# Kernel optimization log

Hardware: AMD Instinct MI355X
Metric: run time of the kernel (lower is better)

The kernel has to match this reference:

```python
import jax, jax.numpy as jnp
import numpy as np

WORD_DIM = 200
ASPECT_DIM = 32
NUM_NEG = 2
AVG_RATING = 3.8
LR_RATING = 1.0
LR_ABAE = 1.0


def setup_inputs() -> dict:
    key = jax.random.key(0)
    ks = jax.random.split(key, 20)
    R, L, D, A, B, NNZ = 20000, 30, WORD_DIM, ASPECT_DIM, 4096, 65536
    e_w = jax.random.normal(ks[0], (R, L, D), jnp.float32)
    y_s = jax.random.normal(ks[1], (R, D), jnp.float32)
    z_n = jax.random.normal(ks[2], (R * NUM_NEG, D), jnp.float32)
    label = jax.random.uniform(ks[3], (B,), jnp.float32, 1.0, 5.0)
    u_idx = jnp.stack([jax.random.randint(ks[4], (NNZ,), 0, B),
                       jax.random.randint(ks[5], (NNZ,), 0, R)]).astype(jnp.int64)
    i_idx = jnp.stack([jax.random.randint(ks[6], (NNZ,), 0, B),
                       jax.random.randint(ks[7], (NNZ,), 0, R)]).astype(jnp.int64)
    u_val = jax.random.uniform(ks[8], (NNZ,), jnp.float32)
    i_val = jax.random.uniform(ks[9], (NNZ,), jnp.float32)
    s = 0.05
    M_w = jax.random.normal(ks[10], (D, D), jnp.float32) * s
    M_b = jnp.zeros((D,), jnp.float32)
    W_w = jax.random.normal(ks[11], (A, D), jnp.float32) * s
    W_b = jnp.zeros((A,), jnp.float32)
    T_w = jax.random.normal(ks[12], (D, A), jnp.float32) * s
    T_b = jnp.zeros((D,), jnp.float32)
    fc_w = jax.random.uniform(ks[13], (1, A), jnp.float32, -0.05, 0.05)
    fc_b = jnp.zeros((1,), jnp.float32)
    fm_V = jax.random.uniform(ks[14], (A, 10), jnp.float32, -0.05, 0.05)
    return dict(e_w=e_w, y_s=y_s, z_n=z_n, label=label,
                user_histor_value=u_val, item_histor_value=i_val,
                M_w=M_w, M_b=M_b, W_w=W_w, W_b=W_b, T_w=T_w, T_b=T_b,
                fc_w=fc_w, fc_b=fc_b, fm_V=fm_V,
                user_histor_index=u_idx, item_histor_index=i_idx)


def _l2norm(x, axis):
    return x / jnp.maximum(jnp.linalg.norm(x, axis=axis, keepdims=True), 1e-12)


def reference(e_w, y_s, z_n, label, user_histor_value, item_histor_value,
              M_w, M_b, W_w, W_b, T_w, T_b, fc_w, fc_b, fm_V,
              user_histor_index, item_histor_index):
    R, L, D = e_w.shape
    A = W_w.shape[0]
    B = label.shape[0]
    # ABAE attention: dx = (e_w @ M^T + b) . y_s  -> (R, L)
    Me = jnp.einsum('rld,ed->rle', e_w, M_w) + M_b  # (R, L, D)
    dx = jnp.einsum('rld,rd->rl', Me, y_s)
    ax = jax.nn.softmax(dx, axis=1)                 # attention over words
    z_s = jnp.einsum('rld,rl->rd', e_w, ax)         # (R, D) weighted sentence emb
    p_t = z_s @ W_w.T + W_b                         # (R, A) aspect weights
    r_s = p_t @ T_w.T + T_b                         # (R, D) reconstructed emb
    # margin ranking (hinge) loss on cosine similarities
    c1 = jnp.sum(_l2norm(r_s, 1) * _l2norm(z_s, 1), axis=-1, keepdims=True)  # (R,1)
    c1 = jnp.tile(c1, (1, NUM_NEG)).reshape(-1)                              # (R*neg,)
    zn = _l2norm(z_n.reshape(R, NUM_NEG, D), 2)
    c2 = jnp.sum(zn * _l2norm(r_s, 1)[:, None, :], axis=-1).reshape(-1)
    abae_out_loss = jnp.maximum(0.0, 1.0 - (c1 - c2))
    J_loss = jnp.mean(abae_out_loss)
    # orthogonality regularizer on aspect matrix columns
    Tn = _l2norm(T_w, 0)                            # normalize each column (dim=0)
    G = Tn.T @ Tn                                   # (A, A)
    U_loss = jnp.mean((G - jnp.eye(A, dtype=G.dtype)) ** 2)
    abae_loss = U_loss + J_loss
    # sparse pooling: (B, R) sparse @ (R, A)
    u_rows, u_cols = user_histor_index[0], user_histor_index[1]
    i_rows, i_cols = item_histor_index[0], item_histor_index[1]
    user_aspect = jax.ops.segment_sum(p_t[u_cols] * user_histor_value[:, None],
                                      u_rows, num_segments=B)
    item_aspect = jax.ops.segment_sum(p_t[i_cols] * item_histor_value[:, None],
                                      i_rows, num_segments=B)
    output_emb = user_aspect * item_aspect          # (B, A)
    # factorization machine
    fm_linear = output_emb @ fc_w.T + fc_b          # (B, 1)
    i1 = (output_emb @ fm_V) ** 2
    i2 = (output_emb ** 2) @ (fm_V ** 2)
    # NOTE: faithful to source -- the 0.5*sum reduces over ALL elements (scalar)
    fm_output = 0.5 * jnp.sum(i1 - i2) + fm_linear  # (B, 1)
    prediction = fm_output + jnp.float32(AVG_RATING)
    rating_out_loss = (prediction.reshape(-1) - label) ** 2
    rating_loss = jnp.mean(rating_out_loss)
    obj = LR_RATING * rating_loss + LR_ABAE * abae_loss
    return (obj, rating_out_loss, abae_out_loss, prediction, user_aspect, item_aspect)
```

## Files before the change

kernel.cpp:

```cpp
#include <hip/hip_runtime.h>
#include <hip/hip_bf16.h>
#include <math.h>

#define R_CNT   20000
#define L_CNT   30
#define D_CNT   200
#define A_CNT   32
#define B_CNT   4096
#define NNZ_CNT 65536
#define AVG_RATING 3.8f

#define KA_GRID 1536

#define OUT_OBJ  0
#define OUT_RL   1
#define OUT_AB   (1 + B_CNT)
#define OUT_PRED (OUT_AB + 2*R_CNT)
#define OUT_UA   (OUT_PRED + B_CNT)
#define OUT_IA   (OUT_UA + B_CNT*A_CNT)

#define WS_DBL    0
#define WS_MODE   32
#define WS_FMLIN  64
#define WS_PT     16448
#define WS_V      2576448
#define WS_JPART  18627648
#define WS_SPART  18667648
#define WS_UPART  18671744

#define BAR_LDS() do { asm volatile("s_waitcnt lgkmcnt(0)" ::: "memory"); \
                       __builtin_amdgcn_s_barrier(); \
                       __builtin_amdgcn_sched_barrier(0); } while (0)
#define BAR_FULL() do { asm volatile("s_waitcnt vmcnt(0) lgkmcnt(0)" ::: "memory"); \
                        __builtin_amdgcn_s_barrier(); \
                        __builtin_amdgcn_sched_barrier(0); } while (0)

__device__ __forceinline__ float4 blk_reduce4(float4 v, float4* scratch) {
    __syncthreads();
    #pragma unroll
    for (int o = 32; o >= 1; o >>= 1) {
        v.x += __shfl_xor(v.x, o);
        v.y += __shfl_xor(v.y, o);
        v.z += __shfl_xor(v.z, o);
        v.w += __shfl_xor(v.w, o);
    }
    int w = threadIdx.x >> 6;
    if ((threadIdx.x & 63) == 0) scratch[w] = v;
    __syncthreads();
    float4 t0 = scratch[0], t1 = scratch[1], t2 = scratch[2], t3 = scratch[3];
    return make_float4(t0.x + t1.x + t2.x + t3.x,
                       t0.y + t1.y + t2.y + t3.y,
                       t0.z + t1.z + t2.z + t3.z,
                       t0.w + t1.w + t2.w + t3.w);
}

__global__ __launch_bounds__(256) void k_pre(const float* __restrict__ y_s,
                                             const float* __restrict__ M_w,
                                             const float* __restrict__ T_w,
                                             const int* __restrict__ u_idx,
                                             float* __restrict__ V,
                                             float* __restrict__ upart,
                                             float* __restrict__ out,
                                             double* __restrict__ dbl,
                                             int* __restrict__ mode) {
    __shared__ __align__(16) float sh[8224];
    const int tid = threadIdx.x;
    const int bid = blockIdx.x;

    if (bid < 313) {
        float* Msh = sh;
        float* Ysh = sh + 6500;
        int r0 = bid * 64;
        int dg = tid & 31, rg = tid >> 5;
        float acc[8][8];
        #pragma unroll
        for (int i = 0; i < 8; i++)
            #pragma unroll
            for (int j = 0; j < 8; j++) acc[i][j] = 0.f;
        for (int e0 = 0; e0 < D_CNT; e0 += 25) {
            __syncthreads();
            for (int idx = tid; idx < 25 * 256; idx += 256) {
                int ee = idx >> 8, d = idx & 255;
                Msh[ee * 260 + d] = (d < D_CNT) ? M_w[(e0 + ee) * D_CNT + d] : 0.f;
            }
            for (int idx = tid; idx < 25 * 64; idx += 256) {
                int rr = idx / 25, ee = idx - rr * 25;
                int row = r0 + rr;
                Ysh[ee * 68 + rr] = (row < R_CNT) ? y_s[row * D_CNT + e0 + ee] : 0.f;
            }
            __syncthreads();
            for (int ee = 0; ee < 25; ee++) {
                const float4 ya = *(const float4*)&Ysh[ee * 68 + rg * 8];
                const float4 yb = *(const float4*)&Ysh[ee * 68 + rg * 8 + 4];
                const float4 ma = *(const float4*)&Msh[ee * 260 + dg * 8];
                const float4 mb = *(const float4*)&Msh[ee * 260 + dg * 8 + 4];
                float ys[8] = {ya.x, ya.y, ya.z, ya.w, yb.x, yb.y, yb.z, yb.w};
                float ms[8] = {ma.x, ma.y, ma.z, ma.w, mb.x, mb.y, mb.z, mb.w};
                #pragma unroll
                for (int i = 0; i < 8; i++)
                    #pragma unroll
                    for (int j = 0; j < 8; j++)
                        acc[i][j] = fmaf(ys[i], ms[j], acc[i][j]);
            }
        }
        if (dg < 25) {
            #pragma unroll
            for (int i = 0; i < 8; i++) {
                int row = r0 + rg * 8 + i;
                if (row < R_CNT) {
                    *(float4*)&V[row * D_CNT + dg * 8]     = make_float4(acc[i][0], acc[i][1], acc[i][2], acc[i][3]);
                    *(float4*)&V[row * D_CNT + dg * 8 + 4] = make_float4(acc[i][4], acc[i][5], acc[i][6], acc[i][7]);
                }
            }
        }
    } else if (bid < 345) {
        float* Tsh = sh;
        float* tn  = sh + 6400;
        float4* red4 = (float4*)(sh + 6448);
        for (int idx = tid; idx < 1600; idx += 256)
            ((float4*)Tsh)[idx] = ((const float4*)T_w)[idx];
        __syncthreads();
        int a = tid >> 3, k = tid & 7;
        float p = 0.f;
        #pragma unroll
        for (int j = 0; j < 25; ++j) { float t = Tsh[(k + 8*j)*32 + a]; p = fmaf(t, t, p); }
        p += __shfl_xor(p, 1); p += __shfl_xor(p, 2); p += __shfl_xor(p, 4);
        if (k == 0) tn[a] = fmaxf(sqrtf(p), 1e-12f);
        __syncthreads();
        const int i = bid - 313;
        float s = 0.f;
        #pragma unroll
        for (int j = 0; j < 25; ++j)
            s = fmaf(Tsh[(k + 8*j)*32 + i], Tsh[(k + 8*j)*32 + a], s);
        s += __shfl_xor(s, 1); s += __shfl_xor(s, 2); s += __shfl_xor(s, 4);
        float part = 0.f;
        if (k == 0) {
            float g = s / (tn[i] * tn[a]);
            float diff = g - ((i == a) ? 1.f : 0.f);
            part = diff * diff;
        }
        float4 tot = blk_reduce4(make_float4(part, 0.f, 0.f, 0.f), red4);
        if (tid == 0) upart[i] = tot.x;
    } else {
        int base = (bid - 345) * 2048;
        #pragma unroll
        for (int j = 0; j < 8; ++j)
            out[OUT_UA + base + j * 256 + tid] = 0.f;
        if (bid == 345 && tid == 0) {
            dbl[0] = 0.0; dbl[1] = 0.0; dbl[2] = 0.0;
            int m = 1;
            for (int i = 1; i < 256; i += 2) if (u_idx[i] != 0) { m = 0; break; }
            *mode = m;
        }
    }
}

__device__ __forceinline__ void stage_E(const float* __restrict__ ew_src,
                                        float* ldsE, int w, int lane) {
    #pragma unroll
    for (int i = 0; i < 6; ++i) {
        int c = w * 6 + i;
        int f4 = c * 64 + lane;
        if (f4 > 1499) f4 = 1499;
        __builtin_amdgcn_global_load_lds(
            (const __attribute__((address_space(1))) unsigned int*)(ew_src + (size_t)f4 * 4),
            (__attribute__((address_space(3))) unsigned int*)(ldsE + c * 256),
            16, 0, 0);
    }
}
__device__ __forceinline__ void stage_V(const float* __restrict__ v_src,
                                        float* ldsV, int w, int lane) {
    __builtin_amdgcn_global_load_lds(
        (const __attribute__((address_space(1))) unsigned int*)(v_src + w * 64 + lane),
        (__attribute__((address_space(3))) unsigned int*)(ldsV + w * 64),
        4, 0, 0);
}

__global__ __launch_bounds__(256, 6) void k_attn(const float* __restrict__ e_w,
                                                 const float* __restrict__ V,
                                                 const float* __restrict__ z_n,
                                                 const float* __restrict__ W_w,
                                                 const float* __restrict__ W_b,
                                                 const float* __restrict__ T_w,
                                                 const float* __restrict__ T_b,
                                                 float* __restrict__ p_t,
                                                 float* __restrict__ out,
                                                 double* __restrict__ jpart) {
    __shared__ __align__(16) float bufE[6144];
    __shared__ __align__(16) float bufV[256];
    __shared__ __align__(16) float zsh[D_CNT];
    __shared__ float axs[32], pts[32];
    __shared__ float4 red[8];
    const int tid = threadIdx.x;
    const int w = tid >> 6, lane = tid & 63;
    const float wb = W_b[tid >> 3];
    const float tb = (tid < D_CNT) ? T_b[tid] : 0.f;
    double jloc = 0.0;

    int r = blockIdx.x;
    stage_E(e_w + (size_t)r * 6000, bufE, w, lane);
    stage_V(V + (size_t)r * D_CNT, bufV, w, lane);
    __syncthreads();

    for (;;) {
        const int rn = r + KA_GRID;
        const bool have_next = (rn < R_CNT);

        float zn0 = 0.f, zn1 = 0.f;
        if (tid < D_CNT) {
            zn0 = z_n[(size_t)(2 * r) * D_CNT + tid];
            zn1 = z_n[(size_t)(2 * r + 1) * D_CNT + tid];
        }

        if (tid < 240) {
            int l = tid >> 3, k = tid & 7;
            float p = 0.f;
            #pragma unroll
            for (int j = 0; j < 25; ++j)
                p = fmaf(bufE[l * 200 + k + 8 * j], bufV[k + 8 * j], p);
            p += __shfl_xor(p, 1); p += __shfl_xor(p, 2); p += __shfl_xor(p, 4);
            if (k == 0) axs[l] = p;
        }
        BAR_LDS();

        if (tid < 64) {
            float v = (tid < L_CNT) ? axs[tid] : -3.0e38f;
            float m = v;
            #pragma unroll
            for (int o = 32; o >= 1; o >>= 1) m = fmaxf(m, __shfl_xor(m, o));
            float e = (tid < L_CNT) ? __expf(v - m) : 0.f;
            float s = e;
            #pragma unroll
            for (int o = 32; o >= 1; o >>= 1) s += __shfl_xor(s, o);
            if (tid < L_CNT) axs[tid] = e / s;
        }
        BAR_LDS();

        float zreg = 0.f;
        if (tid < D_CNT) {
            #pragma unroll
            for (int l = 0; l < L_CNT; ++l)
                zreg = fmaf(bufE[l * 200 + tid], axs[l], zreg);
            zsh[tid] = zreg;
        }
        BAR_LDS();

        if (have_next) {
            stage_E(e_w + (size_t)rn * 6000, bufE, w, lane);
            stage_V(V + (size_t)rn * D_CNT, bufV, w, lane);
        }

        {
            int a = tid >> 3, k = tid & 7;
            float p = 0.f;
            #pragma unroll
            for (int j = 0; j < 25; ++j)
                p = fmaf(zsh[k + 8 * j], W_w[a * 200 + k + 8 * j], p);
            p += __shfl_xor(p, 1); p += __shfl_xor(p, 2); p += __shfl_xor(p, 4);
            if (k == 0) {
                float pt = p + wb;
                pts[a] = pt;
                p_t[(size_t)r * 32 + a] = pt;
            }
        }
        BAR_LDS();

        float rv = 0.f;
        if (tid < D_CNT) {
            rv = tb;
            const float4* tw = (const float4*)(T_w + tid * 32);
            #pragma unroll
            for (int q = 0; q < 8; ++q) {
                float4 t = tw[q];
                rv = fmaf(t.x, pts[4 * q + 0], rv);
                rv = fmaf(t.y, pts[4 * q + 1], rv);
                rv = fmaf(t.z, pts[4 * q + 2], rv);
                rv = fmaf(t.w, pts[4 * q + 3], rv);
            }
        }
        float4 Av = make_float4(rv * rv, rv * zreg, zreg * zreg, zn0 * zn0);
        float4 Bv = make_float4(zn0 * rv, zn1 * zn1, zn1 * rv, 0.f);
        #pragma unroll
        for (int o = 32; o >= 1; o >>= 1) {
            Av.x += __shfl_xor(Av.x, o); Av.y += __shfl_xor(Av.y, o);
            Av.z += __shfl_xor(Av.z, o); Av.w += __shfl_xor(Av.w, o);
            Bv.x += __shfl_xor(Bv.x, o); Bv.y += __shfl_xor(Bv.y, o);
            Bv.z += __shfl_xor(Bv.z, o);
        }
        if ((tid & 63) == 0) { red[2 * w] = Av; red[2 * w + 1] = Bv; }

        BAR_FULL();

        if (tid == 0) {
            float rr = 0.f, rz = 0.f, zz = 0.f, n00 = 0.f, n0r = 0.f, n11 = 0.f, n1r = 0.f;
            #pragma unroll
            for (int i = 0; i < 4; ++i) {
                float4 a = red[2 * i], b = red[2 * i + 1];
                rr += a.x; rz += a.y; zz += a.z; n00 += a.w;
                n0r += b.x; n11 += b.y; n1r += b.z;
            }
            float nr = fmaxf(sqrtf(rr), 1e-12f);
            float nz = fmaxf(sqrtf(zz), 1e-12f);
            float c1  = rz  / (nr * nz);
            float c20 = n0r / (fmaxf(sqrtf(n00), 1e-12f) * nr);
            float c21 = n1r / (fmaxf(sqrtf(n11), 1e-12f) * nr);
            float l0 = fmaxf(0.f, 1.f - (c1 - c20));
            float l1 = fmaxf(0.f, 1.f - (c1 - c21));
            out[OUT_AB + 2 * r]     = l0;
            out[OUT_AB + 2 * r + 1] = l1;
            jloc += (double)l0 + (double)l1;
        }
        if (!have_next) break;
        r = rn;
    }
    if (tid == 0) jpart[blockIdx.x] = jloc;
}

__global__ __launch_bounds__(256) void k_scatter(const int* __restrict__ u_idx,
                                                 const int* __restrict__ i_idx,
                                                 const float* __restrict__ u_val,
                                                 const float* __restrict__ i_val,
                                                 const float* __restrict__ p_t,
                                                 const int* __restrict__ mode,
                                                 float* __restrict__ out) {
    long long gid = (long long)blockIdx.x * 256 + threadIdx.x;
    const long long HALF = (long long)NNZ_CNT * 32;
    int is_item = gid >= HALF;
    long long rem = gid - (is_item ? HALF : 0);
    int k = (int)(rem >> 5), a = (int)(rem & 31);
    const int* idx = is_item ? i_idx : u_idx;
    const float* val = is_item ? i_val : u_val;
    int m64 = *mode;
    int row, col;
    if (m64) { row = idx[2 * k]; col = idx[2 * (NNZ_CNT + k)]; }
    else     { row = idx[k];     col = idx[NNZ_CNT + k]; }
    float v = p_t[col * 32 + a] * val[k];
    float* base = out + (is_item ? OUT_IA : OUT_UA);
    atomicAdd(&base[row * 32 + a], v);
}

__global__ __launch_bounds__(256) void k_fm(const float* __restrict__ out,
                                            const float* __restrict__ fc_w,
                                            const float* __restrict__ fc_b,
                                            const float* __restrict__ fm_V,
                                            float* __restrict__ fm_lin,
                                            double* __restrict__ spart) {
    __shared__ float parts[8];
    int tid = threadIdx.x;
    int a = tid & 31;
    int b = blockIdx.x * 8 + (tid >> 5);
    float ua = out[OUT_UA + b * 32 + a];
    float ia = out[OUT_IA + b * 32 + a];
    float oe = ua * ia;
    float oe2 = oe * oe;
    float lin = oe * fc_w[a];
    #pragma unroll
    for (int o = 1; o < 32; o <<= 1) lin += __shfl_xor(lin, o);
    float part = 0.f;
    #pragma unroll
    for (int j = 0; j < 10; j++) {
        float v = fm_V[a * 10 + j];
        float s1 = oe * v;
        float s2 = oe2 * v * v;
        #pragma unroll
        for (int o = 1; o < 32; o <<= 1) { s1 += __shfl_xor(s1, o); s2 += __shfl_xor(s2, o); }
        part += s1 * s1 - s2;
    }
    if (a == 0) {
        fm_lin[b] = lin + fc_b[0];
        parts[tid >> 5] = part;
    }
    __syncthreads();
    if (tid == 0) {
        float s = 0.f;
        #pragma unroll
        for (int i = 0; i < 8; ++i) s += parts[i];
        spart[blockIdx.x] = 0.5 * (double)s;
    }
}

__global__ __launch_bounds__(256) void k_predfinal(const float* __restrict__ label,
                                                   const float* __restrict__ fm_lin,
                                                   const double* __restrict__ spart,
                                                   const double* __restrict__ jpart,
                                                   const float* __restrict__ upart,
                                                   float* __restrict__ out) {
    __shared__ double dred[4];
    __shared__ float Ssh;
    int tid = threadIdx.x;
    double sl = spart[tid] + spart[tid + 256];
    #pragma unroll
    for (int o = 32; o >= 1; o >>= 1) sl += __shfl_xor(sl, o);
    if ((tid & 63) == 0) dred[tid >> 6] = sl;
    __syncthreads();
    if (tid == 0) Ssh = (float)(dred[0] + dred[1] + dred[2] + dred[3]);
    __syncthreads();
    float S = Ssh;
    double racc = 0.0;
    #pragma unroll
    for (int i = 0; i < 16; ++i) {
        int b = tid + 256 * i;
        float pred = fm_lin[b] + S + AVG_RATING;
        float d = pred - label[b];
        float rl = d * d;
        out[OUT_PRED + b] = pred;
        out[OUT_RL + b] = rl;
        racc += (double)rl;
    }
    double jacc = 0.0;
    for (int i = tid; i < KA_GRID; i += 256) jacc += jpart[i];
    float u = (tid < 32) ? upart[tid] : 0.f;
    #pragma unroll
    for (int o = 32; o >= 1; o >>= 1) {
        racc += __shfl_xor(racc, o);
        jacc += __shfl_xor(jacc, o);
        u    += __shfl_xor(u, o);
    }
    __syncthreads();
    if ((tid & 63) == 0) dred[tid >> 6] = racc;
    __syncthreads();
    double rsum = dred[0] + dred[1] + dred[2] + dred[3];
    __syncthreads();
    if ((tid & 63) == 0) dred[tid >> 6] = jacc;
    __syncthreads();
    double jsum = dred[0] + dred[1] + dred[2] + dred[3];
    __shared__ float ured[4];
    if ((tid & 63) == 0) ured[tid >> 6] = u;
    __syncthreads();
    if (tid == 0) {
        double U = (double)(ured[0] + ured[1] + ured[2] + ured[3]) / 1024.0;
        double J = jsum / (2.0 * R_CNT);
        double RL = rsum / (double)B_CNT;
        out[OUT_OBJ] = (float)(RL + U + J);
    }
}

extern "C" void kernel_launch(void* const* d_in, const int* in_sizes, int n_in,
                              void* d_out, int out_size, void* d_ws, size_t ws_size,
                              hipStream_t stream) {
    const float* e_w   = (const float*)d_in[0];
    const float* y_s   = (const float*)d_in[1];
    const float* z_n   = (const float*)d_in[2];
    const float* label = (const float*)d_in[3];
    const float* u_val = (const float*)d_in[4];
    const float* i_val = (const float*)d_in[5];
    const float* M_w   = (const float*)d_in[6];
    const float* W_w   = (const float*)d_in[8];
    const float* W_b   = (const float*)d_in[9];
    const float* T_w   = (const float*)d_in[10];
    const float* T_b   = (const float*)d_in[11];
    const float* fc_w  = (const float*)d_in[12];
    const float* fc_b  = (const float*)d_in[13];
    const float* fm_V  = (const float*)d_in[14];
    const int*   u_idx = (const int*)d_in[15];
    const int*   i_idx = (const int*)d_in[16];

    float* out = (float*)d_out;
    char* ws = (char*)d_ws;
    double* dbl   = (double*)(ws + WS_DBL);
    int* mode     = (int*)(ws + WS_MODE);
    float* fm_lin = (float*)(ws + WS_FMLIN);
    float* p_t    = (float*)(ws + WS_PT);
    float* V      = (float*)(ws + WS_V);
    double* jpart = (double*)(ws + WS_JPART);
    double* spart = (double*)(ws + WS_SPART);
    float* upart  = (float*)(ws + WS_UPART);

    k_pre<<<473, 256, 0, stream>>>(y_s, M_w, T_w, u_idx, V, upart, out, dbl, mode);
    k_attn<<<KA_GRID, 256, 0, stream>>>(e_w, V, z_n, W_w, W_b, T_w, T_b,
                                        p_t, out, jpart);
    k_scatter<<<(2 * NNZ_CNT * 32) / 256, 256, 0, stream>>>(u_idx, i_idx, u_val, i_val,
                                                            p_t, mode, out);
    k_fm<<<B_CNT / 8, 256, 0, stream>>>(out, fc_w, fc_b, fm_V, fm_lin, spart);
    k_predfinal<<<1, 256, 0, stream>>>(label, fm_lin, spart, jpart, upart, out);
}
```

Baseline: 370.2 us.

## Split attention into streaming online-softmax kernel and batched tail kernel

Replaces the persistent LDS-staged attention kernel with two kernels. The first gives each 64-lane wave one review row: it streams e_w with float4 loads, prefetches the next two positions, and keeps an online softmax so the weighted sum is built in registers, overwriting V with z. The second kernel handles four rows per block for the W/T projections and the hinge loss, reusing each W_w load across the four rows. The aim is more concurrent memory traffic on the dominant e_w read, with fewer block barriers. The cost is an extra launch and a round trip of z through global memory, and only 50 of 64 lanes do useful work in the streaming kernel.

```diff
diff --git a/kernel.cpp b/kernel.cpp
--- a/kernel.cpp
+++ b/kernel.cpp
@@ -10,7 +10,8 @@
 #define NNZ_CNT 65536
 #define AVG_RATING 3.8f
 
-#define KA_GRID 1536
+#define FLASH_GRID 5000
+#define TAIL_GRID  5000
 
 #define OUT_OBJ  0
 #define OUT_RL   1
@@ -27,13 +28,6 @@
 #define WS_JPART  18627648
 #define WS_SPART  18667648
 #define WS_UPART  18671744
-
-#define BAR_LDS() do { asm volatile("s_waitcnt lgkmcnt(0)" ::: "memory"); \
-                       __builtin_amdgcn_s_barrier(); \
-                       __builtin_amdgcn_sched_barrier(0); } while (0)
-#define BAR_FULL() do { asm volatile("s_waitcnt vmcnt(0) lgkmcnt(0)" ::: "memory"); \
-                        __builtin_amdgcn_s_barrier(); \
-                        __builtin_amdgcn_sched_barrier(0); } while (0)
 
 __device__ __forceinline__ float4 blk_reduce4(float4 v, float4* scratch) {
     __syncthreads();
@@ -155,131 +149,136 @@
     }
 }
 
-__device__ __forceinline__ void stage_E(const float* __restrict__ ew_src,
-                                        float* ldsE, int w, int lane) {
-    #pragma unroll
-    for (int i = 0; i < 6; ++i) {
-        int c = w * 6 + i;
-        int f4 = c * 64 + lane;
-        if (f4 > 1499) f4 = 1499;
-        __builtin_amdgcn_global_load_lds(
-            (const __attribute__((address_space(1))) unsigned int*)(ew_src + (size_t)f4 * 4),
-            (__attribute__((address_space(3))) unsigned int*)(ldsE + c * 256),
-            16, 0, 0);
-    }
-}
-__device__ __forceinline__ void stage_V(const float* __restrict__ v_src,
-                                        float* ldsV, int w, int lane) {
-    __builtin_amdgcn_global_load_lds(
-        (const __attribute__((address_space(1))) unsigned int*)(v_src + w * 64 + lane),
-        (__attribute__((address_space(3))) unsigned int*)(ldsV + w * 64),
-        4, 0, 0);
-}
-
-__global__ __launch_bounds__(256, 6) void k_attn(const float* __restrict__ e_w,
-                                                 const float* __restrict__ V,
-                                                 const float* __restrict__ z_n,
-                                                 const float* __restrict__ W_w,
-                                                 const float* __restrict__ W_b,
-                                                 const float* __restrict__ T_w,
-                                                 const float* __restrict__ T_b,
-                                                 float* __restrict__ p_t,
-                                                 float* __restrict__ out,
-                                                 double* __restrict__ jpart) {
-    __shared__ __align__(16) float bufE[6144];
-    __shared__ __align__(16) float bufV[256];
-    __shared__ __align__(16) float zsh[D_CNT];
-    __shared__ float axs[32], pts[32];
+__global__ __launch_bounds__(256, 6) void k_flash(const float* __restrict__ e_w,
+                                                  float* __restrict__ V) {
+    const int lane = threadIdx.x & 63;
+    const int r = blockIdx.x * 4 + (threadIdx.x >> 6);
+    const bool act = lane < 50;
+    const int dl = act ? lane : 0;
+
+    const float4* ew4 = (const float4*)(e_w + (size_t)r * (L_CNT * D_CNT));
+    float4 v4 = ((const float4*)(V + (size_t)r * D_CNT))[dl];
+
+    float m = -3.0e38f, s = 0.f;
+    float4 zs = make_float4(0.f, 0.f, 0.f, 0.f);
+    float4 e0 = ew4[dl];
+    float4 e1 = ew4[50 + dl];
+    #pragma unroll
+    for (int l = 0; l < L_CNT; l += 2) {
+        float4 n0 = e0, n1 = e1;
+        if (l + 2 < L_CNT) {
+            n0 = ew4[(l + 2) * 50 + dl];
+            n1 = ew4[(l + 3) * 50 + dl];
+        }
+        float p0 = act ? (e0.x*v4.x + e0.y*v4.y + e0.z*v4.z + e0.w*v4.w) : 0.f;
+        float p1 = act ? (e1.x*v4.x + e1.y*v4.y + e1.z*v4.z + e1.w*v4.w) : 0.f;
+        #pragma unroll
+        for (int o = 1; o < 64; o <<= 1) {
+            p0 += __shfl_xor(p0, o);
+            p1 += __shfl_xor(p1, o);
+        }
+        float nm = fmaxf(m, fmaxf(p0, p1));
+        float sc = __expf(m - nm);
+        float w0 = __expf(p0 - nm);
+        float w1 = __expf(p1 - nm);
+        s = s * sc + w0 + w1;
+        zs.x = zs.x * sc + w0 * e0.x + w1 * e1.x;
+        zs.y = zs.y * sc + w0 * e0.y + w1 * e1.y;
+        zs.z = zs.z * sc + w0 * e0.z + w1 * e1.z;
+        zs.w = zs.w * sc + w0 * e0.w + w1 * e1.w;
+        m = nm;
+        e0 = n0; e1 = n1;
+    }
+    const float inv = 1.f / s;
+    zs.x *= inv; zs.y *= inv; zs.z *= inv; zs.w *= inv;
+    if (act) ((float4*)(V + (size_t)r * D_CNT))[lane] = zs;
+}
+
+__global__ __launch_bounds__(256) void k_tail(const float* __restrict__ zs,
+                                              const float* __restrict__ z_n,
+                                              const float* __restrict__ W_w,
+                                              const float* __restrict__ W_b,
+                                              const float* __restrict__ T_w,
+                                              const float* __restrict__ T_b,
+                                              float* __restrict__ p_t,
+                                              float* __restrict__ out,
+                                              double* __restrict__ jpart) {
+    __shared__ __align__(16) float zsh[4 * D_CNT];
+    __shared__ float pts[4 * 32];
     __shared__ float4 red[8];
     const int tid = threadIdx.x;
-    const int w = tid >> 6, lane = tid & 63;
-    const float wb = W_b[tid >> 3];
-    const float tb = (tid < D_CNT) ? T_b[tid] : 0.f;
+    const int w = tid >> 6;
+    const int r0 = blockIdx.x * 4;
+
+    for (int i = tid; i < 200; i += 256)
+        ((float4*)zsh)[i] = ((const float4*)(zs + (size_t)r0 * D_CNT))[i];
+
+    float zn[8];
+    #pragma unroll
+    for (int q = 0; q < 8; ++q) zn[q] = 0.f;
+    if (tid < D_CNT) {
+        #pragma unroll
+        for (int q = 0; q < 4; ++q) {
+            zn[2*q]   = z_n[(size_t)(2*(r0+q))     * D_CNT + tid];
+            zn[2*q+1] = z_n[(size_t)(2*(r0+q) + 1) * D_CNT + tid];
+        }
+    }
+    __syncthreads();
+
+    {
+        int a = tid >> 3, k = tid & 7;
+        float a0 = 0.f, a1 = 0.f, a2 = 0.f, a3 = 0.f;
+        #pragma unroll
+        for (int j = 0; j < 25; ++j) {
+            float wv = W_w[a * D_CNT + k + 8 * j];
+            a0 = fmaf(zsh[0*D_CNT + k + 8*j], wv, a0);
+            a1 = fmaf(zsh[1*D_CNT + k + 8*j], wv, a1);
+            a2 = fmaf(zsh[2*D_CNT + k + 8*j], wv, a2);
+            a3 = fmaf(zsh[3*D_CNT + k + 8*j], wv, a3);
+        }
+        #pragma unroll
+        for (int o = 1; o < 8; o <<= 1) {
+            a0 += __shfl_xor(a0, o); a1 += __shfl_xor(a1, o);
+            a2 += __shfl_xor(a2, o); a3 += __shfl_xor(a3, o);
+        }
+        if (k == 0) {
+            float wbv = W_b[a];
+            float p0 = a0 + wbv, p1 = a1 + wbv, p2 = a2 + wbv, p3 = a3 + wbv;
+            pts[0*32+a] = p0; pts[1*32+a] = p1; pts[2*32+a] = p2; pts[3*32+a] = p3;
+            p_t[(size_t)(r0+0) * 32 + a] = p0;
+            p_t[(size_t)(r0+1) * 32 + a] = p1;
+            p_t[(size_t)(r0+2) * 32 + a] = p2;
+            p_t[(size_t)(r0+3) * 32 + a] = p3;
+        }
+    }
+    __syncthreads();
+
+    float rv[4] = {0.f, 0.f, 0.f, 0.f};
+    float zv[4] = {0.f, 0.f, 0.f, 0.f};
+    if (tid < D_CNT) {
+        float tbv = T_b[tid];
+        rv[0] = tbv; rv[1] = tbv; rv[2] = tbv; rv[3] = tbv;
+        const float4* tw = (const float4*)(T_w + tid * 32);
+        #pragma unroll
+        for (int u = 0; u < 8; ++u) {
+            float4 t = tw[u];
+            #pragma unroll
+            for (int q = 0; q < 4; ++q) {
+                rv[q] = fmaf(t.x, pts[q*32 + 4*u + 0], rv[q]);
+                rv[q] = fmaf(t.y, pts[q*32 + 4*u + 1], rv[q]);
+                rv[q] = fmaf(t.z, pts[q*32 + 4*u + 2], rv[q]);
+                rv[q] = fmaf(t.w, pts[q*32 + 4*u + 3], rv[q]);
+            }
+        }
+        #pragma unroll
+        for (int q = 0; q < 4; ++q) zv[q] = zsh[q * D_CNT + tid];
+    }
+
     double jloc = 0.0;
-
-    int r = blockIdx.x;
-    stage_E(e_w + (size_t)r * 6000, bufE, w, lane);
-    stage_V(V + (size_t)r * D_CNT, bufV, w, lane);
-    __syncthreads();
-
-    for (;;) {
-        const int rn = r + KA_GRID;
-        const bool have_next = (rn < R_CNT);
-
-        float zn0 = 0.f, zn1 = 0.f;
-        if (tid < D_CNT) {
-            zn0 = z_n[(size_t)(2 * r) * D_CNT + tid];
-            zn1 = z_n[(size_t)(2 * r + 1) * D_CNT + tid];
-        }
-
-        if (tid < 240) {
-            int l = tid >> 3, k = tid & 7;
-            float p = 0.f;
-            #pragma unroll
-            for (int j = 0; j < 25; ++j)
-                p = fmaf(bufE[l * 200 + k + 8 * j], bufV[k + 8 * j], p);
-            p += __shfl_xor(p, 1); p += __shfl_xor(p, 2); p += __shfl_xor(p, 4);
-            if (k == 0) axs[l] = p;
-        }
-        BAR_LDS();
-
-        if (tid < 64) {
-            float v = (tid < L_CNT) ? axs[tid] : -3.0e38f;
-            float m = v;
-            #pragma unroll
-            for (int o = 32; o >= 1; o >>= 1) m = fmaxf(m, __shfl_xor(m, o));
-            float e = (tid < L_CNT) ? __expf(v - m) : 0.f;
-            float s = e;
-            #pragma unroll
-            for (int o = 32; o >= 1; o >>= 1) s += __shfl_xor(s, o);
-            if (tid < L_CNT) axs[tid] = e / s;
-        }
-        BAR_LDS();
-
-        float zreg = 0.f;
-        if (tid < D_CNT) {
-            #pragma unroll
-            for (int l = 0; l < L_CNT; ++l)
-                zreg = fmaf(bufE[l * 200 + tid], axs[l], zreg);
-            zsh[tid] = zreg;
-        }
-        BAR_LDS();
-
-        if (have_next) {
-            stage_E(e_w + (size_t)rn * 6000, bufE, w, lane);
-            stage_V(V + (size_t)rn * D_CNT, bufV, w, lane);
-        }
-
-        {
-            int a = tid >> 3, k = tid & 7;
-            float p = 0.f;
-            #pragma unroll
-            for (int j = 0; j < 25; ++j)
-                p = fmaf(zsh[k + 8 * j], W_w[a * 200 + k + 8 * j], p);
-            p += __shfl_xor(p, 1); p += __shfl_xor(p, 2); p += __shfl_xor(p, 4);
-            if (k == 0) {
-                float pt = p + wb;
-                pts[a] = pt;
-                p_t[(size_t)r * 32 + a] = pt;
-            }
-        }
-        BAR_LDS();
-
-        float rv = 0.f;
-        if (tid < D_CNT) {
-            rv = tb;
-            const float4* tw = (const float4*)(T_w + tid * 32);
-            #pragma unroll
-            for (int q = 0; q < 8; ++q) {
-                float4 t = tw[q];
-                rv = fmaf(t.x, pts[4 * q + 0], rv);
-                rv = fmaf(t.y, pts[4 * q + 1], rv);
-                rv = fmaf(t.z, pts[4 * q + 2], rv);
-                rv = fmaf(t.w, pts[4 * q + 3], rv);
-            }
-        }
-        float4 Av = make_float4(rv * rv, rv * zreg, zreg * zreg, zn0 * zn0);
-        float4 Bv = make_float4(zn0 * rv, zn1 * zn1, zn1 * rv, 0.f);
+    #pragma unroll
+    for (int q = 0; q < 4; ++q) {
+        float4 Av = make_float4(rv[q]*rv[q], rv[q]*zv[q], zv[q]*zv[q], zn[2*q]*zn[2*q]);
+        float4 Bv = make_float4(zn[2*q]*rv[q], zn[2*q+1]*zn[2*q+1], zn[2*q+1]*rv[q], 0.f);
         #pragma unroll
         for (int o = 32; o >= 1; o >>= 1) {
             Av.x += __shfl_xor(Av.x, o); Av.y += __shfl_xor(Av.y, o);
@@ -287,15 +286,13 @@
             Bv.x += __shfl_xor(Bv.x, o); Bv.y += __shfl_xor(Bv.y, o);
             Bv.z += __shfl_xor(Bv.z, o);
         }
-        if ((tid & 63) == 0) { red[2 * w] = Av; red[2 * w + 1] = Bv; }
-
-        BAR_FULL();
-
+        if ((tid & 63) == 0) { red[2*w] = Av; red[2*w+1] = Bv; }
+        __syncthreads();
         if (tid == 0) {
             float rr = 0.f, rz = 0.f, zz = 0.f, n00 = 0.f, n0r = 0.f, n11 = 0.f, n1r = 0.f;
             #pragma unroll
             for (int i = 0; i < 4; ++i) {
-                float4 a = red[2 * i], b = red[2 * i + 1];
+                float4 a = red[2*i], b = red[2*i+1];
                 rr += a.x; rz += a.y; zz += a.z; n00 += a.w;
                 n0r += b.x; n11 += b.y; n1r += b.z;
             }
@@ -306,12 +303,11 @@
             float c21 = n1r / (fmaxf(sqrtf(n11), 1e-12f) * nr);
             float l0 = fmaxf(0.f, 1.f - (c1 - c20));
             float l1 = fmaxf(0.f, 1.f - (c1 - c21));
-            out[OUT_AB + 2 * r]     = l0;
-            out[OUT_AB + 2 * r + 1] = l1;
+            out[OUT_AB + 2 * (r0 + q)]     = l0;
+            out[OUT_AB + 2 * (r0 + q) + 1] = l1;
             jloc += (double)l0 + (double)l1;
         }
-        if (!have_next) break;
-        r = rn;
+        __syncthreads();
     }
     if (tid == 0) jpart[blockIdx.x] = jloc;
 }
@@ -387,6 +383,7 @@
                                                    float* __restrict__ out) {
     __shared__ double dred[4];
     __shared__ float Ssh;
+    __shared__ float ured[4];
     int tid = threadIdx.x;
     double sl = spart[tid] + spart[tid + 256];
     #pragma unroll
@@ -408,7 +405,7 @@
         racc += (double)rl;
     }
     double jacc = 0.0;
-    for (int i = tid; i < KA_GRID; i += 256) jacc += jpart[i];
+    for (int i = tid; i < TAIL_GRID; i += 256) jacc += jpart[i];
     float u = (tid < 32) ? upart[tid] : 0.f;
     #pragma unroll
     for (int o = 32; o >= 1; o >>= 1) {
@@ -424,7 +421,6 @@
     if ((tid & 63) == 0) dred[tid >> 6] = jacc;
     __syncthreads();
     double jsum = dred[0] + dred[1] + dred[2] + dred[3];
-    __shared__ float ured[4];
     if ((tid & 63) == 0) ured[tid >> 6] = u;
     __syncthreads();
     if (tid == 0) {
@@ -467,8 +463,8 @@
     float* upart  = (float*)(ws + WS_UPART);
 
     k_pre<<<473, 256, 0, stream>>>(y_s, M_w, T_w, u_idx, V, upart, out, dbl, mode);
-    k_attn<<<KA_GRID, 256, 0, stream>>>(e_w, V, z_n, W_w, W_b, T_w, T_b,
-                                        p_t, out, jpart);
+    k_flash<<<FLASH_GRID, 256, 0, stream>>>(e_w, V);
+    k_tail<<<TAIL_GRID, 256, 0, stream>>>(V, z_n, W_w, W_b, T_w, T_b, p_t, out, jpart);
     k_scatter<<<(2 * NNZ_CNT * 32) / 256, 256, 0, stream>>>(u_idx, i_idx, u_val, i_val,
                                                             p_t, mode, out);
     k_fm<<<B_CNT / 8, 256, 0, stream>>>(out, fc_w, fc_b, fm_V, fm_lin, spart);
```

Result: slower. 720.2 us (+94.6%).
